# Kernel tuning notes

Measured on AMD Instinct MI355X. Metric: run time of the kernel, lower is better.

The kernel has to match this reference:

```python
import jax, jax.numpy as jnp
import numpy as np

N_NODES = 100000
NINP = 128
N_EDGES = 1600000
EPS = 1e-12


def _gcn_conv(x, W, b, src, dst, deg_inv_sqrt):
    # PyG GCNConv: h = x W; out = D^{-1/2}(A+I)D^{-1/2} h + b
    h = x @ W  # [N, out_dim]
    norm = deg_inv_sqrt[src] * deg_inv_sqrt[dst]  # [E]
    agg = jax.ops.segment_sum(h[src] * norm[:, None], dst, num_segments=N_NODES)
    # self-loop contribution: weight deg_inv_sqrt[i]^2
    agg = agg + h * (deg_inv_sqrt ** 2)[:, None]
    return agg + b


def setup_inputs() -> dict:
    key = jax.random.key(0)
    k1, k2, k3, k4 = jax.random.split(key, 4)
    edge_index = jax.random.randint(k1, (2, N_EDGES), 0, N_NODES, dtype=jnp.int64)
    # embedding table (xavier-normal-like), padding_idx=0 row zeroed
    emb = jax.random.normal(k2, (N_NODES, NINP), dtype=jnp.float32) * (2.0 / (N_NODES + NINP)) ** 0.5
    emb = emb.at[0].set(0.0)
    W1 = jax.random.normal(k3, (NINP, 2 * NINP), dtype=jnp.float32) * (1.0 / NINP) ** 0.5
    b1 = jnp.zeros((2 * NINP,), dtype=jnp.float32)
    W2 = jax.random.normal(k4, (2 * NINP, NINP), dtype=jnp.float32) * (1.0 / (2 * NINP)) ** 0.5
    b2 = jnp.zeros((NINP,), dtype=jnp.float32)
    return {"emb": emb, "W1": W1, "b1": b1, "W2": W2, "b2": b2, "edge_index": edge_index}


def reference(emb, W1, b1, W2, b2, edge_index):
    src, dst = edge_index[0], edge_index[1]
    # symmetric GCN degree with self-loops (in-degree on dst + 1)
    deg = jax.ops.segment_sum(jnp.ones_like(dst, dtype=emb.dtype), dst, num_segments=N_NODES) + 1.0
    deg_inv_sqrt = jax.lax.rsqrt(deg)
    x = _gcn_conv(emb, W1, b1, src, dst, deg_inv_sqrt)  # [N, 2*ninp]
    # F.normalize(p=2, dim=-1)
    x = x / jnp.maximum(jnp.linalg.norm(x, axis=-1, keepdims=True), EPS)
    # dropout in eval mode (identity)
    out = _gcn_conv(x, W2, b2, src, dst, deg_inv_sqrt)  # [N, ninp]
    return out
```

## Files before the change

### kernel.cpp

```cpp
#include <hip/hip_runtime.h>
#include <hip/hip_bf16.h>

typedef __attribute__((ext_vector_type(8))) short bf16x8;
typedef __attribute__((ext_vector_type(4))) float f32x4;

#define NBUCK 391
#define BCAP 8192


__device__ __forceinline__ ushort f2bf(float f) {
    unsigned int b = __float_as_uint(f);
    unsigned int r = (b + 0x7fffu + ((b >> 16) & 1u)) >> 16;
    return (ushort)r;
}
__device__ __forceinline__ float bflo(uint v) { return __uint_as_float(v << 16); }
__device__ __forceinline__ float bfhi(uint v) { return __uint_as_float(v & 0xffff0000u); }


__global__ __launch_bounds__(256) void bucket_kernel(const int* __restrict__ src, const int* __restrict__ dst,
                                                     int* __restrict__ gcur, int2* __restrict__ pairs,
                                                     int E, int chunk,
                                                     const float* __restrict__ W1, ushort* __restrict__ W1t,
                                                     const float* __restrict__ W2, ushort* __restrict__ W2t) {
    int b = blockIdx.x, t = threadIdx.x;
    if (b >= 512) {
        if (b < 640) {
            int i = (b - 512) * 256 + t;
            int n = i >> 7, k = i & 127;
            W1t[i] = f2bf(W1[(size_t)k * 256 + n]);
        } else {
            int i = (b - 640) * 256 + t;
            int n = i >> 8, k = i & 255;
            W2t[i] = f2bf(W2[(size_t)k * 128 + n]);
        }
        return;
    }
    __shared__ int lcnt[NBUCK];
    for (int q = t; q < NBUCK; q += 256) lcnt[q] = 0;
    __syncthreads();
    int e0 = b * chunk;
    int e1 = e0 + chunk; if (e1 > E) e1 = E;
    for (int e = e0 + t; e < e1; e += 256)
        atomicAdd(&lcnt[dst[e] >> 8], 1);
    __syncthreads();
    for (int q = t; q < NBUCK; q += 256) {
        int c = lcnt[q];
        lcnt[q] = c ? atomicAdd(&gcur[q], c) : 0;
    }
    __syncthreads();
    for (int e = e0 + t; e < e1; e += 256) {
        int d = dst[e], s = src[e];
        int bb = d >> 8;
        int p = atomicAdd(&lcnt[bb], 1);
        if (p < BCAP) pairs[(size_t)bb * BCAP + p] = make_int2(d, s);
    }
}


__global__ __launch_bounds__(512) void scan_buckets(const int* __restrict__ gcur, int* __restrict__ bbase,
                                                    int* __restrict__ offs, int Nn, int E) {
    int i = threadIdx.x;
    int v = (i < NBUCK) ? min(gcur[i], BCAP) : 0;
    int lane = i & 63, wid = i >> 6;
    int x = v;
#pragma unroll
    for (int d = 1; d < 64; d <<= 1) {
        int y = __shfl_up(x, d, 64);
        if (lane >= d) x += y;
    }
    __shared__ int wsum[8], wpre[8];
    if (lane == 63) wsum[wid] = x;
    __syncthreads();
    if (i == 0) {
        int run = 0;
        for (int w = 0; w < 8; ++w) { wpre[w] = run; run += wsum[w]; }
        offs[Nn] = E;
    }
    __syncthreads();
    if (i < NBUCK) bbase[i] = x - v + wpre[wid];
}


__global__ __launch_bounds__(256) void csr_kernel(const int2* __restrict__ pairs, const int* __restrict__ gcur,
                                                  const int* __restrict__ bbase,
                                                  int* __restrict__ offs, float* __restrict__ dis,
                                                  int* __restrict__ csr,
                                                  const float4* __restrict__ emb4, ushort4* __restrict__ tbl4,
                                                  int Nn) {
    int b = blockIdx.x;
    int n0 = b << 8;
    int ne = min(gcur[b], BCAP);
    __shared__ int cnt[256], off[256], pos[256];
    __shared__ float sdis[256];
    int i = threadIdx.x;
    cnt[i] = 0;
    __syncthreads();
    const int2* pp = pairs + (size_t)b * BCAP;
    for (int e = i; e < ne; e += 256)
        atomicAdd(&cnt[pp[e].x - n0], 1);
    __syncthreads();
    int lane = i & 63, wid = i >> 6;
    int v = cnt[i];
    int x = v;
#pragma unroll
    for (int d = 1; d < 64; d <<= 1) {
        int y = __shfl_up(x, d, 64);
        if (lane >= d) x += y;
    }
    __shared__ int wsum[4], wpre[4];
    if (lane == 63) wsum[wid] = x;
    __syncthreads();
    if (i == 0) {
        int run = 0;
        for (int w = 0; w < 4; ++w) { wpre[w] = run; run += wsum[w]; }
    }
    __syncthreads();
    int excl = x - v + wpre[wid];
    off[i] = excl;
    pos[i] = 0;
    int n = n0 + i;
    float s = rsqrtf((float)v + 1.0f);
    sdis[i] = s;
    if (n < Nn) {
        offs[n] = bbase[b] + excl;
        dis[n] = s;
    }
    __syncthreads();
    int base = bbase[b];
    for (int e = i; e < ne; e += 256) {
        int2 r = pp[e];
        int li = r.x - n0;
        int p = atomicAdd(&pos[li], 1);
        csr[base + off[li] + p] = r.y;
    }
    for (int q = i; q < 256 * 32; q += 256) {
        int rw = q >> 5;
        int nn = n0 + rw;
        if (nn < Nn) {
            float sc = sdis[rw];
            float4 vv = emb4[(size_t)nn * 32 + (q & 31)];
            ushort4 o;
            o.x = f2bf(vv.x * sc); o.y = f2bf(vv.y * sc);
            o.z = f2bf(vv.z * sc); o.w = f2bf(vv.w * sc);
            tbl4[(size_t)nn * 32 + (q & 31)] = o;
        }
    }
}


template <bool BIAS, bool BF16OUT>
__global__ __launch_bounds__(256) void agg2x(const uint2* __restrict__ tbl2x,
                                             const int* __restrict__ offs,
                                             const int* __restrict__ rec,
                                             const float* __restrict__ dis,
                                             const float* __restrict__ bias,
                                             void* __restrict__ outp, int Nn) {
    int wave = (int)((blockIdx.x * 256 + threadIdx.x) >> 6);
    int lane = threadIdx.x & 63;
    int i31 = lane & 31;
    int gw = wave * 2 + (lane >> 5);
    bool valid = gw < Nn;
    int gc = valid ? gw : Nn - 1;
    float dn = dis[gc];
    int e0 = offs[gc], e1 = offs[gc + 1];
    int eclamp = (e1 > 0) ? e1 - 1 : 0;
    uint2 hv = tbl2x[(size_t)gc * 32 + i31];
    float a0 = bflo(hv.x), a1 = bfhi(hv.x), a2 = bflo(hv.y), a3 = bfhi(hv.y);

    for (int base = e0; __any(base < e1); base += 8) {
        int ee = base + (i31 & 7);
        uint rr = (uint)rec[ee < e1 ? ee : eclamp];
        uint ix[8];
#pragma unroll
        for (int j = 0; j < 8; ++j) ix[j] = (uint)__shfl((int)rr, j, 32);
        uint2 vv[8];
#pragma unroll
        for (int j = 0; j < 8; ++j) vv[j] = tbl2x[(size_t)ix[j] * 32u + (uint)i31];
#pragma unroll
        for (int j = 0; j < 8; ++j) {
            bool ok = (base + j) < e1;
            uint xx = ok ? vv[j].x : 0u;
            uint yy = ok ? vv[j].y : 0u;
            a0 += bflo(xx); a1 += bfhi(xx);
            a2 += bflo(yy); a3 += bfhi(yy);
        }
    }

    a0 *= dn; a1 *= dn; a2 *= dn; a3 *= dn;
    if (BIAS) {
        float4 bv = reinterpret_cast<const float4*>(bias)[i31];
        a0 += bv.x; a1 += bv.y; a2 += bv.z; a3 += bv.w;
    }
    if (valid) {
        if (BF16OUT) {
            uint2 o;
            o.x = (uint)f2bf(a0) | ((uint)f2bf(a1) << 16);
            o.y = (uint)f2bf(a2) | ((uint)f2bf(a3) << 16);
            reinterpret_cast<uint2*>(outp)[(size_t)gw * 32 + i31] = o;
        } else {
            float4 o = make_float4(a0, a1, a2, a3);
            reinterpret_cast<float4*>(outp)[(size_t)gw * 32 + i31] = o;
        }
    }
}


__global__ __launch_bounds__(512, 4) void fused_gemm(const ushort* __restrict__ A,
                                                     const ushort* __restrict__ W1t,
                                                     const float* __restrict__ bias1,
                                                     const ushort* __restrict__ W2t,
                                                     const float* __restrict__ dsc,
                                                     ushort* __restrict__ out2, int M) {
    __shared__ __align__(16) ushort sA[64 * 128];
    __shared__ __align__(16) ushort xt[64 * 256];
    __shared__ float ssl[8][64];
    int tid = threadIdx.x;
    int lane = tid & 63, wid = tid >> 6;
    int g = lane >> 4, i15 = lane & 15;
    int koff = g * 8;
    int m0 = blockIdx.x * 64;

    {
        const char* Ab = reinterpret_cast<const char*>(A);
        char* sAb = reinterpret_cast<char*>(sA);
#pragma unroll
        for (int j = 0; j < 2; ++j) {
            int byte = j * 8192 + tid * 16;
            int row = byte >> 8;
            int grow = m0 + row; if (grow >= M) grow = M - 1;
            bf16x8 v = *reinterpret_cast<const bf16x8*>(Ab + (size_t)grow * 256 + (byte & 255));
            *reinterpret_cast<bf16x8*>(sAb + (byte ^ ((row & 7) << 4))) = v;
        }
    }

    bf16x8 b1f[2][4];
    float bv[2];
#pragma unroll
    for (int ns = 0; ns < 2; ++ns) {
        int c = wid * 32 + ns * 16 + i15;
        const bf16x8* p = reinterpret_cast<const bf16x8*>(W1t + (size_t)c * 128 + koff);
#pragma unroll
        for (int ks = 0; ks < 4; ++ks) b1f[ns][ks] = p[ks * 4];
        bv[ns] = bias1[c];
    }
    __syncthreads();

    const char* sAb = reinterpret_cast<const char*>(sA);
    f32x4 acc[4][2];
#pragma unroll
    for (int ms = 0; ms < 4; ++ms)
#pragma unroll
        for (int ns = 0; ns < 2; ++ns) acc[ms][ns] = (f32x4){0.f, 0.f, 0.f, 0.f};
#pragma unroll
    for (int ks = 0; ks < 4; ++ks) {
        bf16x8 a[4];
#pragma unroll
        for (int ms = 0; ms < 4; ++ms) {
            int row = ms * 16 + i15;
            int byte = row * 256 + ks * 64 + g * 16;
            a[ms] = *reinterpret_cast<const bf16x8*>(sAb + (byte ^ ((row & 7) << 4)));
        }
#pragma unroll
        for (int ms = 0; ms < 4; ++ms)
#pragma unroll
            for (int ns = 0; ns < 2; ++ns)
                acc[ms][ns] = __builtin_amdgcn_mfma_f32_16x16x32_bf16(a[ms], b1f[ns][ks], acc[ms][ns], 0, 0, 0);
    }

    float ps[4][4];
#pragma unroll
    for (int ms = 0; ms < 4; ++ms)
#pragma unroll
        for (int r = 0; r < 4; ++r) {
            float s = 0.f;
#pragma unroll
            for (int ns = 0; ns < 2; ++ns) {
                float v = acc[ms][ns][r] + bv[ns];
                acc[ms][ns][r] = v;
                s += v * v;
            }
            ps[ms][r] = s;
        }
#pragma unroll
    for (int d = 1; d < 16; d <<= 1)
#pragma unroll
        for (int ms = 0; ms < 4; ++ms)
#pragma unroll
            for (int r = 0; r < 4; ++r) ps[ms][r] += __shfl_xor(ps[ms][r], d, 64);
    if (i15 == 0) {
#pragma unroll
        for (int ms = 0; ms < 4; ++ms)
#pragma unroll
            for (int r = 0; r < 4; ++r) ssl[wid][ms * 16 + g * 4 + r] = ps[ms][r];
    }
    __syncthreads();

#pragma unroll
    for (int ms = 0; ms < 4; ++ms)
#pragma unroll
        for (int r = 0; r < 4; ++r) {
            int rt = ms * 16 + g * 4 + r;
            float tot = 0.f;
#pragma unroll
            for (int w = 0; w < 8; ++w) tot += ssl[w][rt];
            float inv = 1.0f / fmaxf(sqrtf(tot), 1e-12f);
            int sw = (rt & 7) << 3;
#pragma unroll
            for (int ns = 0; ns < 2; ++ns) {
                int col = wid * 32 + ns * 16 + i15;
                xt[(rt * 256 + col) ^ sw] = f2bf(acc[ms][ns][r] * inv);
            }
        }
    __syncthreads();

    bf16x8 b2f[8];
    {
        int c = wid * 16 + i15;
        const bf16x8* p = reinterpret_cast<const bf16x8*>(W2t + (size_t)c * 256 + koff);
#pragma unroll
        for (int ks = 0; ks < 8; ++ks) b2f[ks] = p[ks * 4];
    }

    f32x4 acc2[4];
#pragma unroll
    for (int ms = 0; ms < 4; ++ms) acc2[ms] = (f32x4){0.f, 0.f, 0.f, 0.f};
#pragma unroll
    for (int ks = 0; ks < 8; ++ks) {
        bf16x8 a2[4];
#pragma unroll
        for (int ms = 0; ms < 4; ++ms) {
            int rowA = ms * 16 + i15;
            int eb = (rowA * 256 + koff + ks * 32) ^ ((rowA & 7) << 3);
            a2[ms] = *reinterpret_cast<const bf16x8*>(&xt[eb]);
        }
#pragma unroll
        for (int ms = 0; ms < 4; ++ms)
            acc2[ms] = __builtin_amdgcn_mfma_f32_16x16x32_bf16(a2[ms], b2f[ks], acc2[ms], 0, 0, 0);
    }

#pragma unroll
    for (int ms = 0; ms < 4; ++ms)
#pragma unroll
        for (int r = 0; r < 4; ++r) {
            int row = m0 + ms * 16 + g * 4 + r;
            if (row < M) {
                float sc = dsc[row];
                out2[(size_t)row * 128 + wid * 16 + i15] = f2bf(acc2[ms][r] * sc);
            }
        }
}


extern "C" void kernel_launch(void* const* d_in, const int* in_sizes, int n_in,
                              void* d_out, int out_size, void* d_ws, size_t ws_size,
                              hipStream_t stream) {
    const float* emb = (const float*)d_in[0];
    const float* W1 = (const float*)d_in[1];
    const float* b1 = (const float*)d_in[2];
    const float* W2 = (const float*)d_in[3];
    const float* b2 = (const float*)d_in[4];
    const int* eidx = (const int*)d_in[5];

    const int Nn = in_sizes[0] / 128;
    const int E = in_sizes[5] / 2;
    const int* srcp = eidx;
    const int* dstp = eidx + E;

    float* ws = (float*)d_ws;
    size_t o = 0;
    uint* tbl1 = (uint*)(ws + o);  o += (size_t)Nn * 64;
    uint* axb = (uint*)(ws + o);   o += (size_t)Nn * 64;
    uint* tbl2 = (uint*)(ws + o);  o += (size_t)Nn * 64;
    ushort* W1t = (ushort*)(ws + o); o += 128 * 256 / 2;
    ushort* W2t = (ushort*)(ws + o); o += 256 * 128 / 2;
    float* dis = ws + o;    o += Nn;
    int* gcur = (int*)(ws + o);   o += NBUCK + 1;
    int* bbase = (int*)(ws + o);  o += NBUCK + 1;
    int* offs = (int*)(ws + o);   o += Nn + 16;
    int* csr = (int*)(ws + o);    o += E;
    int2* pairs = (int2*)(ws + o); o += (size_t)NBUCK * BCAP * 2;

    hipMemsetAsync(gcur, 0, (NBUCK + 1) * sizeof(int), stream);

    int B1B = 512;
    int chunk = (E + B1B - 1) / B1B;
    bucket_kernel<<<768, 256, 0, stream>>>(srcp, dstp, gcur, pairs, E, chunk, W1, W1t, W2, W2t);
    scan_buckets<<<1, 512, 0, stream>>>(gcur, bbase, offs, Nn, E);
    csr_kernel<<<NBUCK, 256, 0, stream>>>(pairs, gcur, bbase, offs, dis, csr,
                                          (const float4*)emb, (ushort4*)tbl1, Nn);

    agg2x<false, true><<<(Nn + 7) / 8, 256, 0, stream>>>((const uint2*)tbl1, offs, csr, dis, nullptr, axb, Nn);
    fused_gemm<<<(Nn + 63) / 64, 512, 0, stream>>>((const ushort*)axb, W1t, b1, W2t, dis, (ushort*)tbl2, Nn);

    agg2x<true, false><<<(Nn + 7) / 8, 256, 0, stream>>>((const uint2*)tbl2, offs, csr, dis, b2, d_out, Nn);
}
```

Before: 233.8 us.

## Pack bucket pairs into 32-bit words, fold bucket scan into CSR kernel, pad zero row

Bucket entries now store the local destination (8 bits) and source (24 bits) in one uint instead of an int2, which halves the scatter and gather traffic of the pairs array. The separate single-block scan kernel is removed; each CSR block sums the preceding bucket counts itself, saving a launch at the cost of some redundant reads of gcur. The aggregation kernels point out-of-range edges at a zeroed padding row, so the per-edge masking selects go away. The packing assumes node ids fit in 24 bits.

```diff
diff --git a/kernel.cpp b/kernel.cpp
--- a/kernel.cpp
+++ b/kernel.cpp
@@ -18,20 +18,23 @@
 
 
 __global__ __launch_bounds__(256) void bucket_kernel(const int* __restrict__ src, const int* __restrict__ dst,
-                                                     int* __restrict__ gcur, int2* __restrict__ pairs,
+                                                     int* __restrict__ gcur, uint* __restrict__ pairs,
                                                      int E, int chunk,
                                                      const float* __restrict__ W1, ushort* __restrict__ W1t,
-                                                     const float* __restrict__ W2, ushort* __restrict__ W2t) {
+                                                     const float* __restrict__ W2, ushort* __restrict__ W2t,
+                                                     uint* __restrict__ tbl1z, uint* __restrict__ tbl2z) {
     int b = blockIdx.x, t = threadIdx.x;
     if (b >= 512) {
         if (b < 640) {
             int i = (b - 512) * 256 + t;
             int n = i >> 7, k = i & 127;
             W1t[i] = f2bf(W1[(size_t)k * 256 + n]);
-        } else {
+        } else if (b < 768) {
             int i = (b - 640) * 256 + t;
             int n = i >> 8, k = i & 255;
             W2t[i] = f2bf(W2[(size_t)k * 128 + n]);
+        } else {
+            if (t < 64) { tbl1z[t] = 0u; tbl2z[t] = 0u; }
         }
         return;
     }
@@ -49,57 +52,42 @@
     }
     __syncthreads();
     for (int e = e0 + t; e < e1; e += 256) {
-        int d = dst[e], s = src[e];
+        int d = dst[e];
+        uint s = (uint)src[e];
         int bb = d >> 8;
         int p = atomicAdd(&lcnt[bb], 1);
-        if (p < BCAP) pairs[(size_t)bb * BCAP + p] = make_int2(d, s);
-    }
-}
-
-
-__global__ __launch_bounds__(512) void scan_buckets(const int* __restrict__ gcur, int* __restrict__ bbase,
-                                                    int* __restrict__ offs, int Nn, int E) {
-    int i = threadIdx.x;
-    int v = (i < NBUCK) ? min(gcur[i], BCAP) : 0;
-    int lane = i & 63, wid = i >> 6;
-    int x = v;
-#pragma unroll
-    for (int d = 1; d < 64; d <<= 1) {
-        int y = __shfl_up(x, d, 64);
-        if (lane >= d) x += y;
-    }
-    __shared__ int wsum[8], wpre[8];
-    if (lane == 63) wsum[wid] = x;
-    __syncthreads();
-    if (i == 0) {
-        int run = 0;
-        for (int w = 0; w < 8; ++w) { wpre[w] = run; run += wsum[w]; }
-        offs[Nn] = E;
-    }
-    __syncthreads();
-    if (i < NBUCK) bbase[i] = x - v + wpre[wid];
-}
-
-
-__global__ __launch_bounds__(256) void csr_kernel(const int2* __restrict__ pairs, const int* __restrict__ gcur,
-                                                  const int* __restrict__ bbase,
+        if (p < BCAP) pairs[(size_t)bb * BCAP + p] = ((uint)(d & 255) << 24) | s;
+    }
+}
+
+
+__global__ __launch_bounds__(256) void csr_kernel(const uint* __restrict__ pairs, const int* __restrict__ gcur,
                                                   int* __restrict__ offs, float* __restrict__ dis,
                                                   int* __restrict__ csr,
                                                   const float4* __restrict__ emb4, ushort4* __restrict__ tbl4,
-                                                  int Nn) {
+                                                  int Nn, int E) {
     int b = blockIdx.x;
     int n0 = b << 8;
     int ne = min(gcur[b], BCAP);
     __shared__ int cnt[256], off[256], pos[256];
     __shared__ float sdis[256];
+    __shared__ int wred[4];
     int i = threadIdx.x;
+    int lane = i & 63, wid = i >> 6;
+
+    int partial = 0;
+    for (int q = i; q < b; q += 256) partial += min(gcur[q], BCAP);
+#pragma unroll
+    for (int d = 1; d < 64; d <<= 1) partial += __shfl_xor(partial, d, 64);
+    if (lane == 0) wred[wid] = partial;
     cnt[i] = 0;
     __syncthreads();
-    const int2* pp = pairs + (size_t)b * BCAP;
+    int base = wred[0] + wred[1] + wred[2] + wred[3];
+
+    const uint* pp = pairs + (size_t)b * BCAP;
     for (int e = i; e < ne; e += 256)
-        atomicAdd(&cnt[pp[e].x - n0], 1);
-    __syncthreads();
-    int lane = i & 63, wid = i >> 6;
+        atomicAdd(&cnt[pp[e] >> 24], 1);
+    __syncthreads();
     int v = cnt[i];
     int x = v;
 #pragma unroll
@@ -122,16 +110,16 @@
     float s = rsqrtf((float)v + 1.0f);
     sdis[i] = s;
     if (n < Nn) {
-        offs[n] = bbase[b] + excl;
+        offs[n] = base + excl;
         dis[n] = s;
     }
-    __syncthreads();
-    int base = bbase[b];
+    if (b == 0 && i == 0) offs[Nn] = E;
+    __syncthreads();
     for (int e = i; e < ne; e += 256) {
-        int2 r = pp[e];
-        int li = r.x - n0;
+        uint r = pp[e];
+        int li = (int)(r >> 24);
         int p = atomicAdd(&pos[li], 1);
-        csr[base + off[li] + p] = r.y;
+        csr[base + off[li] + p] = (int)(r & 0xFFFFFFu);
     }
     for (int q = i; q < 256 * 32; q += 256) {
         int rw = q >> 5;
@@ -163,26 +151,23 @@
     int gc = valid ? gw : Nn - 1;
     float dn = dis[gc];
     int e0 = offs[gc], e1 = offs[gc + 1];
-    int eclamp = (e1 > 0) ? e1 - 1 : 0;
+    uint ZR = (uint)Nn;
     uint2 hv = tbl2x[(size_t)gc * 32 + i31];
     float a0 = bflo(hv.x), a1 = bfhi(hv.x), a2 = bflo(hv.y), a3 = bfhi(hv.y);
 
     for (int base = e0; __any(base < e1); base += 8) {
         int ee = base + (i31 & 7);
-        uint rr = (uint)rec[ee < e1 ? ee : eclamp];
+        uint myidx = (ee < e1) ? (uint)rec[ee] : ZR;
         uint ix[8];
 #pragma unroll
-        for (int j = 0; j < 8; ++j) ix[j] = (uint)__shfl((int)rr, j, 32);
+        for (int j = 0; j < 8; ++j) ix[j] = (uint)__shfl((int)myidx, j, 32);
         uint2 vv[8];
 #pragma unroll
         for (int j = 0; j < 8; ++j) vv[j] = tbl2x[(size_t)ix[j] * 32u + (uint)i31];
 #pragma unroll
         for (int j = 0; j < 8; ++j) {
-            bool ok = (base + j) < e1;
-            uint xx = ok ? vv[j].x : 0u;
-            uint yy = ok ? vv[j].y : 0u;
-            a0 += bflo(xx); a1 += bfhi(xx);
-            a2 += bflo(yy); a3 += bfhi(yy);
+            a0 += bflo(vv[j].x); a1 += bfhi(vv[j].x);
+            a2 += bflo(vv[j].y); a3 += bfhi(vv[j].y);
         }
     }
 
@@ -368,26 +353,25 @@
 
     float* ws = (float*)d_ws;
     size_t o = 0;
-    uint* tbl1 = (uint*)(ws + o);  o += (size_t)Nn * 64;
+    uint* tbl1 = (uint*)(ws + o);  o += (size_t)(Nn + 1) * 64;
     uint* axb = (uint*)(ws + o);   o += (size_t)Nn * 64;
-    uint* tbl2 = (uint*)(ws + o);  o += (size_t)Nn * 64;
+    uint* tbl2 = (uint*)(ws + o);  o += (size_t)(Nn + 1) * 64;
     ushort* W1t = (ushort*)(ws + o); o += 128 * 256 / 2;
     ushort* W2t = (ushort*)(ws + o); o += 256 * 128 / 2;
     float* dis = ws + o;    o += Nn;
     int* gcur = (int*)(ws + o);   o += NBUCK + 1;
-    int* bbase = (int*)(ws + o);  o += NBUCK + 1;
     int* offs = (int*)(ws + o);   o += Nn + 16;
     int* csr = (int*)(ws + o);    o += E;
-    int2* pairs = (int2*)(ws + o); o += (size_t)NBUCK * BCAP * 2;
+    uint* pairs = (uint*)(ws + o); o += (size_t)NBUCK * BCAP;
 
     hipMemsetAsync(gcur, 0, (NBUCK + 1) * sizeof(int), stream);
 
     int B1B = 512;
     int chunk = (E + B1B - 1) / B1B;
-    bucket_kernel<<<768, 256, 0, stream>>>(srcp, dstp, gcur, pairs, E, chunk, W1, W1t, W2, W2t);
-    scan_buckets<<<1, 512, 0, stream>>>(gcur, bbase, offs, Nn, E);
-    csr_kernel<<<NBUCK, 256, 0, stream>>>(pairs, gcur, bbase, offs, dis, csr,
-                                          (const float4*)emb, (ushort4*)tbl1, Nn);
+    bucket_kernel<<<769, 256, 0, stream>>>(srcp, dstp, gcur, pairs, E, chunk, W1, W1t, W2, W2t,
+                                           tbl1 + (size_t)Nn * 64, tbl2 + (size_t)Nn * 64);
+    csr_kernel<<<NBUCK, 256, 0, stream>>>(pairs, gcur, offs, dis, csr,
+                                          (const float4*)emb, (ushort4*)tbl1, Nn, E);
 
     agg2x<false, true><<<(Nn + 7) / 8, 256, 0, stream>>>((const uint2*)tbl1, offs, csr, dis, nullptr, axb, Nn);
     fused_gemm<<<(Nn + 63) / 64, 512, 0, stream>>>((const ushort*)axb, W1t, b1, W2t, dis, (ushort*)tbl2, Nn);
```

New measurement: 229.4 us. About the same (-1.9%).
